# Optimization experiments

Hardware: AMD Instinct MI355X
Metric: run time of the kernel (lower is better)

The kernel has to match this reference:

```python
import jax, jax.numpy as jnp
import numpy as np


def setup_inputs() -> dict:
    key = jax.random.key(0)
    ks = jax.random.split(key, 10)
    B, N, F, H = 4, 512, 64, 4
    x = jax.random.normal(ks[0], (B, N, F), dtype=jnp.float32)
    adj = jax.random.uniform(ks[1], (N, N), dtype=jnp.float32)
    s = 1.0 / np.sqrt(F)
    Wq = jax.random.normal(ks[2], (F, F * H), dtype=jnp.float32) * s
    bq = jnp.zeros((F * H,), dtype=jnp.float32)
    Wk = jax.random.normal(ks[3], (F, F * H), dtype=jnp.float32) * s
    bk = jnp.zeros((F * H,), dtype=jnp.float32)
    Wlin = jax.random.normal(ks[4], (H, F), dtype=jnp.float32) * (1.0 / np.sqrt(H))
    blin = jnp.zeros((F,), dtype=jnp.float32)
    Wfc = jax.random.normal(ks[5], (F, F), dtype=jnp.float32) * s
    bfc = jnp.zeros((F,), dtype=jnp.float32)
    return {"x": x, "adj": adj, "Wq": Wq, "bq": bq, "Wk": Wk, "bk": bk,
            "Wlin": Wlin, "blin": blin, "Wfc": Wfc, "bfc": bfc}


def reference(x, adj, Wq, bq, Wk, bk, Wlin, blin, Wfc, bfc):
    B, N, F = x.shape
    H = Wlin.shape[0]
    # multi-head attention matrix (value projection is computed but unused in the original)
    q = (x @ Wq + bq).reshape(B, N, H, F)  # [B,N,H,F]
    k = (x @ Wk + bk).reshape(B, N, H, F)
    scores = jnp.einsum('bihf,bjhf->bhij', q, k) / jnp.sqrt(jnp.float32(F))
    attn = jax.nn.softmax(scores, axis=-1)  # [B,H,N,N]
    # linear over heads: [B,N,N,H] @ [H,F] -> [B,N,N,F]
    SV2 = jnp.einsum('bhij,hf->bijf', attn, Wlin) + blin
    # symmetric normalization of (adj + I)
    A = adj + jnp.eye(N, dtype=adj.dtype)
    d = jnp.sum(A, axis=1) ** -0.5
    noradj = d[:, None] * A * d[None, :]  # [N,N]
    # sum over dim 1 (source index i) of noradj[i,j]*SV2[b,i,j,f]*x[b,j,f]
    S = jnp.einsum('ij,bijf->bjf', noradj, SV2)
    sx = x * S  # [B,N,F]
    out = jnp.einsum('ij,bjf->bif', noradj, sx)
    out = out @ Wfc + bfc
    return jax.nn.relu(out)
```

## Files before the change

kernel.cpp:

```cpp
#include <hip/hip_runtime.h>
#include <math.h>

#define NN 512
#define FF 64
#define HH 4


__global__ __launch_bounds__(512) void k_s1(const float* __restrict__ x,
                                            const float* __restrict__ Wq,
                                            const float* __restrict__ bq,
                                            const float* __restrict__ Wk,
                                            const float* __restrict__ bk,
                                            const float* __restrict__ adj,
                                            float* __restrict__ q_t,
                                            float* __restrict__ kT,
                                            float* __restrict__ dinv,
                                            float* __restrict__ T,
                                            float* __restrict__ cvec) {
    __shared__ float x_lds[4][64];
    int blk = blockIdx.x, tid = threadIdx.x;
    int wave = tid >> 6, lane = tid & 63;
    int b = blk >> 7, itile = blk & 127;
    int i0 = itile * 4;

    if (wave >= 4) {
        int idx = tid - 256;
        x_lds[idx >> 6][idx & 63] = x[((long)b * NN + i0 + (idx >> 6)) * FF + (idx & 63)];
    } else if (wave == 0) {
        float acc = 0.f;
#pragma unroll
        for (int k = 0; k < 8; ++k) acc += adj[blk * NN + k * 64 + lane];
        for (int o = 32; o > 0; o >>= 1) acc += __shfl_xor(acc, o);
        if (lane == 0) dinv[blk] = 1.0f / sqrtf(acc + 1.0f);
    } else if (wave == 1) {
        if (lane < 16) T[blk * 16 + lane] = 0.f;
    } else if (wave == 2) {
        if (lane == 0) cvec[blk] = 0.f;
    }
    __syncthreads();

    int isK = tid >> 8, col = tid & 255;
    const float* W = isK ? Wk : Wq;
    float bv = (isK ? bk : bq)[col];
    float a0 = bv, a1 = bv, a2 = bv, a3 = bv;
#pragma unroll 8
    for (int cc = 0; cc < 64; ++cc) {
        float w = W[cc * 256 + col];
        a0 = fmaf(x_lds[0][cc], w, a0);
        a1 = fmaf(x_lds[1][cc], w, a1);
        a2 = fmaf(x_lds[2][cc], w, a2);
        a3 = fmaf(x_lds[3][cc], w, a3);
    }
    int h = col >> 6, f = col & 63;
    int bh = b * HH + h;
    if (!isK) {
        long base = ((long)bh * NN + i0) * FF + f;
        q_t[base] = a0; q_t[base + FF] = a1;
        q_t[base + 2 * FF] = a2; q_t[base + 3 * FF] = a3;
    } else {
        long base = ((long)bh * FF + f) * NN + i0;
        *(float4*)(kT + base) = make_float4(a0, a1, a2, a3);
    }
}

__global__ __launch_bounds__(512) void k_s2(const float* __restrict__ q_t,
                                            const float* __restrict__ kT,
                                            const float* __restrict__ adj,
                                            const float* __restrict__ dinv,
                                            float* __restrict__ T,
                                            float* __restrict__ cvec) {
    __shared__ float q_lds[8][64];
    __shared__ float red[8][8];
    __shared__ float red2[8][8];
    int blk = blockIdx.x, tid = threadIdx.x;
    int itile = blk & 63, h = (blk >> 6) & 3, b = blk >> 8;
    int bh = b * HH + h, i0 = itile * 8;
    int wv = tid >> 6, lane = tid & 63;

    q_lds[tid >> 6][tid & 63] = q_t[((long)bh * NN + i0 + (tid >> 6)) * FF + (tid & 63)];
    __syncthreads();

    int j = tid;
    const float* kb = kT + (long)bh * FF * NN;
    float s[8];
#pragma unroll
    for (int r = 0; r < 8; ++r) s[r] = 0.f;
#pragma unroll 2
    for (int f4 = 0; f4 < 64; f4 += 4) {
        float kv[4];
#pragma unroll
        for (int u = 0; u < 4; ++u) kv[u] = kb[(f4 + u) * NN + j];
#pragma unroll
        for (int r = 0; r < 8; ++r) {
            float4 qv = *(const float4*)&q_lds[r][f4];
            s[r] = fmaf(qv.x, kv[0], s[r]);
            s[r] = fmaf(qv.y, kv[1], s[r]);
            s[r] = fmaf(qv.z, kv[2], s[r]);
            s[r] = fmaf(qv.w, kv[3], s[r]);
        }
    }
    const float scale = 0.125f;
#pragma unroll
    for (int r = 0; r < 8; ++r) {
        float v = s[r];
        for (int o = 32; o > 0; o >>= 1) v = fmaxf(v, __shfl_xor(v, o));
        if (lane == 0) red[r][wv] = v;
    }
    __syncthreads();
    float m[8];
#pragma unroll
    for (int r = 0; r < 8; ++r) {
        float v = red[r][0];
#pragma unroll
        for (int w = 1; w < 8; ++w) v = fmaxf(v, red[r][w]);
        m[r] = v;
    }
#pragma unroll
    for (int r = 0; r < 8; ++r) {
        s[r] = expf((s[r] - m[r]) * scale);
        float v = s[r];
        for (int o = 32; o > 0; o >>= 1) v += __shfl_xor(v, o);
        if (lane == 0) red2[r][wv] = v;
    }
    __syncthreads();
    float Zi[8];
#pragma unroll
    for (int r = 0; r < 8; ++r) {
        float v = red2[r][0];
#pragma unroll
        for (int w = 1; w < 8; ++w) v += red2[r][w];
        Zi[r] = 1.0f / v;
    }
    float dj = dinv[j];
    float pw = 0.f, cw = 0.f;
#pragma unroll
    for (int r = 0; r < 8; ++r) {
        int gi = i0 + r;
        float di = dinv[gi];
        float a = adj[(long)gi * NN + j] + (gi == j ? 1.f : 0.f);
        float t = di * a;
        pw = fmaf(t, s[r] * Zi[r], pw);
        cw += t;
    }
    atomicAdd(&T[bh * NN + j], pw * dj);
    if (b == 0 && h == 0) atomicAdd(&cvec[j], cw);
}

__global__ __launch_bounds__(256) void k_s3(const float* __restrict__ x,
                                            const float* __restrict__ T,
                                            const float* __restrict__ Wlin,
                                            const float* __restrict__ blin,
                                            const float* __restrict__ cvec,
                                            const float* __restrict__ adj,
                                            const float* __restrict__ dinv,
                                            const float* __restrict__ Wfc,
                                            const float* __restrict__ bfc,
                                            float* __restrict__ out) {
    __shared__ float4 u4_l[NN];
    __shared__ float  u0_l[NN];
    __shared__ float2 ad_l[NN];
    __shared__ float part[4][2][64];
    __shared__ float m_lds[2][64];
    __shared__ float part2[4][2][64];
    int blk = blockIdx.x, tid = threadIdx.x;
    int b = blk >> 8, itile = blk & 255;
    int i0 = itile * 2;

    for (int jj = tid; jj < NN; jj += 256) {
        float dj = dinv[jj];
        u0_l[jj] = dj * dj * cvec[jj];
        u4_l[jj] = make_float4(dj * T[(b * HH + 0) * NN + jj],
                               dj * T[(b * HH + 1) * NN + jj],
                               dj * T[(b * HH + 2) * NN + jj],
                               dj * T[(b * HH + 3) * NN + jj]);
        ad_l[jj] = make_float2(adj[(long)i0 * NN + jj] + (i0 == jj ? 1.f : 0.f),
                               adj[(long)(i0 + 1) * NN + jj] + (i0 + 1 == jj ? 1.f : 0.f));
    }
    __syncthreads();

    int f = tid & 63, jc = tid >> 6;
    int jb = jc * 128;
    float blf = blin[f];
    float4 wl = make_float4(Wlin[f], Wlin[64 + f], Wlin[128 + f], Wlin[192 + f]);
    const float* xb = x + (long)b * NN * FF + f;
    float a0 = 0.f, a1 = 0.f;
#pragma unroll 4
    for (int j = jb; j < jb + 128; ++j) {
        float xv = xb[(long)j * FF];
        float4 u = u4_l[j];
        float2 ad = ad_l[j];
        float S = blf * u0_l[j];
        S = fmaf(wl.x, u.x, S);
        S = fmaf(wl.y, u.y, S);
        S = fmaf(wl.z, u.z, S);
        S = fmaf(wl.w, u.w, S);
        float sx = xv * S;
        a0 = fmaf(ad.x, sx, a0);
        a1 = fmaf(ad.y, sx, a1);
    }
    part[jc][0][f] = a0;
    part[jc][1][f] = a1;
    __syncthreads();
    if (jc == 0) {
        m_lds[0][f] = (part[0][0][f] + part[1][0][f] + part[2][0][f] + part[3][0][f]) * dinv[i0];
        m_lds[1][f] = (part[0][1][f] + part[1][1][f] + part[2][1][f] + part[3][1][f]) * dinv[i0 + 1];
    }
    __syncthreads();
    float o0 = 0.f, o1 = 0.f;
    int c0 = jc * 16;
#pragma unroll
    for (int cc = 0; cc < 16; ++cc) {
        float w = Wfc[(c0 + cc) * FF + f];
        o0 = fmaf(m_lds[0][c0 + cc], w, o0);
        o1 = fmaf(m_lds[1][c0 + cc], w, o1);
    }
    part2[jc][0][f] = o0;
    part2[jc][1][f] = o1;
    __syncthreads();
    if (jc == 0) {
        float bb = bfc[f];
        float r0 = part2[0][0][f] + part2[1][0][f] + part2[2][0][f] + part2[3][0][f] + bb;
        float r1 = part2[0][1][f] + part2[1][1][f] + part2[2][1][f] + part2[3][1][f] + bb;
        out[((long)b * NN + i0) * FF + f]     = fmaxf(r0, 0.f);
        out[((long)b * NN + i0 + 1) * FF + f] = fmaxf(r1, 0.f);
    }
}

extern "C" void kernel_launch(void* const* d_in, const int* in_sizes, int n_in,
                              void* d_out, int out_size, void* d_ws, size_t ws_size,
                              hipStream_t stream) {
    const float* x    = (const float*)d_in[0];
    const float* adj  = (const float*)d_in[1];
    const float* Wq   = (const float*)d_in[2];
    const float* bq   = (const float*)d_in[3];
    const float* Wk   = (const float*)d_in[4];
    const float* bk   = (const float*)d_in[5];
    const float* Wlin = (const float*)d_in[6];
    const float* blin = (const float*)d_in[7];
    const float* Wfc  = (const float*)d_in[8];
    const float* bfc  = (const float*)d_in[9];
    float* out = (float*)d_out;

    float* ws   = (float*)d_ws;
    float* dinv = ws;
    float* cvec = ws + 512;
    float* T    = ws + 1024;
    float* q_t  = ws + 9216;
    float* kT   = ws + 2106368;

    k_s1<<<dim3(512), dim3(512), 0, stream>>>(x, Wq, bq, Wk, bk, adj, q_t, kT, dinv, T, cvec);
    k_s2<<<dim3(1024), dim3(512), 0, stream>>>(q_t, kT, adj, dinv, T, cvec);
    k_s3<<<dim3(1024), dim3(256), 0, stream>>>(x, T, Wlin, blin, cvec, adj, dinv, Wfc, bfc, out);
}
```

Baseline: 117.2 us.

## Restructure all three stages with register-held weights and row-major K

```diff
diff --git a/kernel.cpp b/kernel.cpp
--- a/kernel.cpp
+++ b/kernel.cpp
@@ -13,23 +13,19 @@
                                             const float* __restrict__ bk,
                                             const float* __restrict__ adj,
                                             float* __restrict__ q_t,
-                                            float* __restrict__ kT,
+                                            float* __restrict__ k_t,
                                             float* __restrict__ dinv,
                                             float* __restrict__ T,
                                             float* __restrict__ cvec) {
-    __shared__ float x_lds[4][64];
     int blk = blockIdx.x, tid = threadIdx.x;
     int wave = tid >> 6, lane = tid & 63;
     int b = blk >> 7, itile = blk & 127;
     int i0 = itile * 4;
 
-    if (wave >= 4) {
-        int idx = tid - 256;
-        x_lds[idx >> 6][idx & 63] = x[((long)b * NN + i0 + (idx >> 6)) * FF + (idx & 63)];
-    } else if (wave == 0) {
+    if (wave == 0) {
         float acc = 0.f;
 #pragma unroll
-        for (int k = 0; k < 8; ++k) acc += adj[blk * NN + k * 64 + lane];
+        for (int k = 0; k < 8; ++k) acc += adj[(long)blk * NN + k * 64 + lane];
         for (int o = 32; o > 0; o >>= 1) acc += __shfl_xor(acc, o);
         if (lane == 0) dinv[blk] = 1.0f / sqrtf(acc + 1.0f);
     } else if (wave == 1) {
@@ -37,113 +33,110 @@
     } else if (wave == 2) {
         if (lane == 0) cvec[blk] = 0.f;
     }
-    __syncthreads();
 
     int isK = tid >> 8, col = tid & 255;
     const float* W = isK ? Wk : Wq;
+    float wv[64];
+#pragma unroll
+    for (int cc = 0; cc < 64; ++cc) wv[cc] = W[cc * 256 + col];
+
     float bv = (isK ? bk : bq)[col];
     float a0 = bv, a1 = bv, a2 = bv, a3 = bv;
-#pragma unroll 8
+    const float* xr = x + ((long)b * NN + i0) * FF;
+#pragma unroll
     for (int cc = 0; cc < 64; ++cc) {
-        float w = W[cc * 256 + col];
-        a0 = fmaf(x_lds[0][cc], w, a0);
-        a1 = fmaf(x_lds[1][cc], w, a1);
-        a2 = fmaf(x_lds[2][cc], w, a2);
-        a3 = fmaf(x_lds[3][cc], w, a3);
+        float w = wv[cc];
+        a0 = fmaf(xr[cc], w, a0);
+        a1 = fmaf(xr[64 + cc], w, a1);
+        a2 = fmaf(xr[128 + cc], w, a2);
+        a3 = fmaf(xr[192 + cc], w, a3);
     }
     int h = col >> 6, f = col & 63;
-    int bh = b * HH + h;
-    if (!isK) {
-        long base = ((long)bh * NN + i0) * FF + f;
-        q_t[base] = a0; q_t[base + FF] = a1;
-        q_t[base + 2 * FF] = a2; q_t[base + 3 * FF] = a3;
-    } else {
-        long base = ((long)bh * FF + f) * NN + i0;
-        *(float4*)(kT + base) = make_float4(a0, a1, a2, a3);
-    }
+    float* dst = (isK ? k_t : q_t) + ((long)(b * HH + h) * NN + i0) * FF + f;
+    dst[0] = a0; dst[FF] = a1; dst[2 * FF] = a2; dst[3 * FF] = a3;
 }
 
 __global__ __launch_bounds__(512) void k_s2(const float* __restrict__ q_t,
-                                            const float* __restrict__ kT,
+                                            const float* __restrict__ k_t,
                                             const float* __restrict__ adj,
                                             const float* __restrict__ dinv,
                                             float* __restrict__ T,
                                             float* __restrict__ cvec) {
-    __shared__ float q_lds[8][64];
-    __shared__ float red[8][8];
-    __shared__ float red2[8][8];
+    __shared__ float red[16][8];
+    __shared__ float red2[16][8];
     int blk = blockIdx.x, tid = threadIdx.x;
-    int itile = blk & 63, h = (blk >> 6) & 3, b = blk >> 8;
-    int bh = b * HH + h, i0 = itile * 8;
-    int wv = tid >> 6, lane = tid & 63;
-
-    q_lds[tid >> 6][tid & 63] = q_t[((long)bh * NN + i0 + (tid >> 6)) * FF + (tid & 63)];
-    __syncthreads();
-
+    int itile = blk & 31, h = (blk >> 5) & 3, b = blk >> 7;
+    int bh = b * HH + h, i0 = itile * 16;
+    int wv_ = tid >> 6, lane = tid & 63;
     int j = tid;
-    const float* kb = kT + (long)bh * FF * NN;
-    float s[8];
-#pragma unroll
-    for (int r = 0; r < 8; ++r) s[r] = 0.f;
-#pragma unroll 2
-    for (int f4 = 0; f4 < 64; f4 += 4) {
-        float kv[4];
-#pragma unroll
-        for (int u = 0; u < 4; ++u) kv[u] = kb[(f4 + u) * NN + j];
-#pragma unroll
-        for (int r = 0; r < 8; ++r) {
-            float4 qv = *(const float4*)&q_lds[r][f4];
-            s[r] = fmaf(qv.x, kv[0], s[r]);
-            s[r] = fmaf(qv.y, kv[1], s[r]);
-            s[r] = fmaf(qv.z, kv[2], s[r]);
-            s[r] = fmaf(qv.w, kv[3], s[r]);
+
+    float4 kv[16];
+    const float4* kb4 = (const float4*)(k_t + ((long)bh * NN + j) * FF);
+#pragma unroll
+    for (int u = 0; u < 16; ++u) kv[u] = kb4[u];
+
+    const float4* qb4 = (const float4*)(q_t + ((long)bh * NN + i0) * FF);
+    float s[16];
+#pragma unroll
+    for (int r = 0; r < 16; ++r) {
+        float acc = 0.f;
+#pragma unroll
+        for (int u = 0; u < 16; ++u) {
+            float4 qv = qb4[r * 16 + u];
+            acc = fmaf(qv.x, kv[u].x, acc);
+            acc = fmaf(qv.y, kv[u].y, acc);
+            acc = fmaf(qv.z, kv[u].z, acc);
+            acc = fmaf(qv.w, kv[u].w, acc);
         }
-    }
+        s[r] = acc;
+    }
+
     const float scale = 0.125f;
 #pragma unroll
-    for (int r = 0; r < 8; ++r) {
+    for (int r = 0; r < 16; ++r) {
         float v = s[r];
         for (int o = 32; o > 0; o >>= 1) v = fmaxf(v, __shfl_xor(v, o));
-        if (lane == 0) red[r][wv] = v;
-    }
-    __syncthreads();
-    float m[8];
-#pragma unroll
-    for (int r = 0; r < 8; ++r) {
+        if (lane == 0) red[r][wv_] = v;
+    }
+    __syncthreads();
+    float m[16];
+#pragma unroll
+    for (int r = 0; r < 16; ++r) {
         float v = red[r][0];
 #pragma unroll
         for (int w = 1; w < 8; ++w) v = fmaxf(v, red[r][w]);
         m[r] = v;
     }
 #pragma unroll
-    for (int r = 0; r < 8; ++r) {
+    for (int r = 0; r < 16; ++r) {
         s[r] = expf((s[r] - m[r]) * scale);
         float v = s[r];
         for (int o = 32; o > 0; o >>= 1) v += __shfl_xor(v, o);
-        if (lane == 0) red2[r][wv] = v;
-    }
-    __syncthreads();
-    float Zi[8];
-#pragma unroll
-    for (int r = 0; r < 8; ++r) {
-        float v = red2[r][0];
-#pragma unroll
-        for (int w = 1; w < 8; ++w) v += red2[r][w];
-        Zi[r] = 1.0f / v;
-    }
+        if (lane == 0) red2[r][wv_] = v;
+    }
+    __syncthreads();
+
+    float av[16];
+#pragma unroll
+    for (int r = 0; r < 16; ++r) av[r] = adj[(long)(i0 + r) * NN + j];
+
     float dj = dinv[j];
     float pw = 0.f, cw = 0.f;
 #pragma unroll
-    for (int r = 0; r < 8; ++r) {
+    for (int r = 0; r < 16; ++r) {
+        float z = red2[r][0];
+#pragma unroll
+        for (int w = 1; w < 8; ++w) z += red2[r][w];
+        float Zi = 1.0f / z;
         int gi = i0 + r;
         float di = dinv[gi];
-        float a = adj[(long)gi * NN + j] + (gi == j ? 1.f : 0.f);
+        float a = av[r] + (gi == j ? 1.f : 0.f);
         float t = di * a;
-        pw = fmaf(t, s[r] * Zi[r], pw);
+        pw = fmaf(t, s[r] * Zi, pw);
         cw += t;
     }
     atomicAdd(&T[bh * NN + j], pw * dj);
-    if (b == 0 && h == 0) atomicAdd(&cvec[j], cw);
+    if (bh == 0) atomicAdd(&cvec[j], cw);
 }
 
 __global__ __launch_bounds__(256) void k_s3(const float* __restrict__ x,
@@ -156,74 +149,60 @@
                                             const float* __restrict__ Wfc,
                                             const float* __restrict__ bfc,
                                             float* __restrict__ out) {
-    __shared__ float4 u4_l[NN];
-    __shared__ float  u0_l[NN];
-    __shared__ float2 ad_l[NN];
-    __shared__ float part[4][2][64];
-    __shared__ float m_lds[2][64];
-    __shared__ float part2[4][2][64];
+    __shared__ float part[4][4][64];
+    __shared__ float m_lds[4][64];
     int blk = blockIdx.x, tid = threadIdx.x;
-    int b = blk >> 8, itile = blk & 255;
-    int i0 = itile * 2;
-
-    for (int jj = tid; jj < NN; jj += 256) {
-        float dj = dinv[jj];
-        u0_l[jj] = dj * dj * cvec[jj];
-        u4_l[jj] = make_float4(dj * T[(b * HH + 0) * NN + jj],
-                               dj * T[(b * HH + 1) * NN + jj],
-                               dj * T[(b * HH + 2) * NN + jj],
-                               dj * T[(b * HH + 3) * NN + jj]);
-        ad_l[jj] = make_float2(adj[(long)i0 * NN + jj] + (i0 == jj ? 1.f : 0.f),
-                               adj[(long)(i0 + 1) * NN + jj] + (i0 + 1 == jj ? 1.f : 0.f));
-    }
-    __syncthreads();
-
+    int b = blk >> 7, itile = blk & 127;
+    int i0 = itile * 4;
     int f = tid & 63, jc = tid >> 6;
     int jb = jc * 128;
+
     float blf = blin[f];
     float4 wl = make_float4(Wlin[f], Wlin[64 + f], Wlin[128 + f], Wlin[192 + f]);
     const float* xb = x + (long)b * NN * FF + f;
-    float a0 = 0.f, a1 = 0.f;
-#pragma unroll 4
-    for (int j = jb; j < jb + 128; ++j) {
-        float xv = xb[(long)j * FF];
-        float4 u = u4_l[j];
-        float2 ad = ad_l[j];
-        float S = blf * u0_l[j];
-        S = fmaf(wl.x, u.x, S);
-        S = fmaf(wl.y, u.y, S);
-        S = fmaf(wl.z, u.z, S);
-        S = fmaf(wl.w, u.w, S);
-        float sx = xv * S;
-        a0 = fmaf(ad.x, sx, a0);
-        a1 = fmaf(ad.y, sx, a1);
-    }
-    part[jc][0][f] = a0;
-    part[jc][1][f] = a1;
-    __syncthreads();
-    if (jc == 0) {
-        m_lds[0][f] = (part[0][0][f] + part[1][0][f] + part[2][0][f] + part[3][0][f]) * dinv[i0];
-        m_lds[1][f] = (part[0][1][f] + part[1][1][f] + part[2][1][f] + part[3][1][f]) * dinv[i0 + 1];
-    }
-    __syncthreads();
-    float o0 = 0.f, o1 = 0.f;
-    int c0 = jc * 16;
-#pragma unroll
-    for (int cc = 0; cc < 16; ++cc) {
-        float w = Wfc[(c0 + cc) * FF + f];
-        o0 = fmaf(m_lds[0][c0 + cc], w, o0);
-        o1 = fmaf(m_lds[1][c0 + cc], w, o1);
-    }
-    part2[jc][0][f] = o0;
-    part2[jc][1][f] = o1;
-    __syncthreads();
-    if (jc == 0) {
-        float bb = bfc[f];
-        float r0 = part2[0][0][f] + part2[1][0][f] + part2[2][0][f] + part2[3][0][f] + bb;
-        float r1 = part2[0][1][f] + part2[1][1][f] + part2[2][1][f] + part2[3][1][f] + bb;
-        out[((long)b * NN + i0) * FF + f]     = fmaxf(r0, 0.f);
-        out[((long)b * NN + i0 + 1) * FF + f] = fmaxf(r1, 0.f);
-    }
+    const float* Tb = T + (long)b * HH * NN;
+    float a0 = 0.f, a1 = 0.f, a2 = 0.f, a3 = 0.f;
+
+    for (int j = jb; j < jb + 128; j += 8) {
+        float xv[8];
+#pragma unroll
+        for (int u = 0; u < 8; ++u) xv[u] = xb[(long)(j + u) * FF];
+#pragma unroll
+        for (int u = 0; u < 8; ++u) {
+            int jj = j + u;
+            float dj = dinv[jj];
+            float cj = dj * dj * cvec[jj];
+            float t0 = dj * Tb[jj];
+            float t1 = dj * Tb[NN + jj];
+            float t2 = dj * Tb[2 * NN + jj];
+            float t3 = dj * Tb[3 * NN + jj];
+            float S = blf * cj;
+            S = fmaf(wl.x, t0, S);
+            S = fmaf(wl.y, t1, S);
+            S = fmaf(wl.z, t2, S);
+            S = fmaf(wl.w, t3, S);
+            float sx = xv[u] * S;
+            float d0 = adj[(long)(i0 + 0) * NN + jj] + (i0 + 0 == jj ? 1.f : 0.f);
+            float d1 = adj[(long)(i0 + 1) * NN + jj] + (i0 + 1 == jj ? 1.f : 0.f);
+            float d2 = adj[(long)(i0 + 2) * NN + jj] + (i0 + 2 == jj ? 1.f : 0.f);
+            float d3 = adj[(long)(i0 + 3) * NN + jj] + (i0 + 3 == jj ? 1.f : 0.f);
+            a0 = fmaf(d0, sx, a0);
+            a1 = fmaf(d1, sx, a1);
+            a2 = fmaf(d2, sx, a2);
+            a3 = fmaf(d3, sx, a3);
+        }
+    }
+    part[jc][0][f] = a0; part[jc][1][f] = a1;
+    part[jc][2][f] = a2; part[jc][3][f] = a3;
+    __syncthreads();
+    m_lds[jc][f] = (part[0][jc][f] + part[1][jc][f] + part[2][jc][f] + part[3][jc][f])
+                   * dinv[i0 + jc];
+    __syncthreads();
+    float o = bfc[f];
+#pragma unroll
+    for (int cc = 0; cc < 64; ++cc)
+        o = fmaf(m_lds[jc][cc], Wfc[cc * FF + f], o);
+    out[((long)b * NN + i0 + jc) * FF + f] = fmaxf(o, 0.f);
 }
 
 extern "C" void kernel_launch(void* const* d_in, const int* in_sizes, int n_in,
@@ -246,9 +225,9 @@
     float* cvec = ws + 512;
     float* T    = ws + 1024;
     float* q_t  = ws + 9216;
-    float* kT   = ws + 2106368;
-
-    k_s1<<<dim3(512), dim3(512), 0, stream>>>(x, Wq, bq, Wk, bk, adj, q_t, kT, dinv, T, cvec);
-    k_s2<<<dim3(1024), dim3(512), 0, stream>>>(q_t, kT, adj, dinv, T, cvec);
-    k_s3<<<dim3(1024), dim3(256), 0, stream>>>(x, T, Wlin, blin, cvec, adj, dinv, Wfc, bfc, out);
-}
+    float* k_t  = ws + 2106368;
+
+    k_s1<<<dim3(512), dim3(512), 0, stream>>>(x, Wq, bq, Wk, bk, adj, q_t, k_t, dinv, T, cvec);
+    k_s2<<<dim3(512), dim3(512), 0, stream>>>(q_t, k_t, adj, dinv, T, cvec);
+    k_s3<<<dim3(512), dim3(256), 0, stream>>>(x, T, Wlin, blin, cvec, adj, dinv, Wfc, bfc, out);
+}
```

After: 145.4 us. +24.1%, slower.
